# Kernel tuning notes

Measured on AMD Instinct MI355X. Metric: run time of the kernel, lower is better.

## Reference

```python
import jax, jax.numpy as jnp
import numpy as np

N = 500_000
IN_CH = 64
OUT_CH = 32
HEADS = 4
NUM_SEGS = 1024


def setup_inputs() -> dict:
    key = jax.random.key(0)
    ks = jax.random.split(key, 8)
    x = jax.random.normal(ks[0], (N, IN_CH), dtype=jnp.float32)
    batch = jnp.sort(jax.random.randint(ks[1], (N,), 0, NUM_SEGS, dtype=jnp.int32))
    batch = batch.at[-1].set(NUM_SEGS - 1)  # mimic size = batch[-1]+1 == NUM_SEGS
    s_in = 1.0 / np.sqrt(IN_CH)
    s_hg = 1.0 / np.sqrt(HEADS * IN_CH)
    s_hm = 1.0 / np.sqrt(OUT_CH * HEADS)
    # gate_nn: Linear(in, heads*in, bias=False) -> PReLU -> Linear(heads*in, heads, bias=False)
    gate_w1 = jax.random.uniform(ks[2], (HEADS * IN_CH, IN_CH), jnp.float32, -s_in, s_in)
    prelu_a = jnp.asarray(0.25, dtype=jnp.float32)
    gate_w2 = jax.random.uniform(ks[3], (HEADS, HEADS * IN_CH), jnp.float32, -s_hg, s_hg)
    # nn: Linear(in, out*heads) -> ReLU -> Linear(out*heads, out*heads)
    mlp_w1 = jax.random.uniform(ks[4], (OUT_CH * HEADS, IN_CH), jnp.float32, -s_in, s_in)
    mlp_b1 = jax.random.uniform(ks[5], (OUT_CH * HEADS,), jnp.float32, -s_in, s_in)
    mlp_w2 = jax.random.uniform(ks[6], (OUT_CH * HEADS, OUT_CH * HEADS), jnp.float32, -s_hm, s_hm)
    mlp_b2 = jax.random.uniform(ks[7], (OUT_CH * HEADS,), jnp.float32, -s_hm, s_hm)
    return {"x": x, "batch": batch, "num_segments": NUM_SEGS,
            "gate_w1": gate_w1, "prelu_a": prelu_a, "gate_w2": gate_w2,
            "mlp_w1": mlp_w1, "mlp_b1": mlp_b1, "mlp_w2": mlp_w2, "mlp_b2": mlp_b2}


def reference(x, batch, num_segments, gate_w1, prelu_a, gate_w2,
              mlp_w1, mlp_b1, mlp_w2, mlp_b2):
    n = x.shape[0]
    # gate network: [N, heads]
    h = x @ gate_w1.T
    h = jnp.where(h >= 0, h, prelu_a * h)  # PReLU (shared scalar slope)
    gate = h @ gate_w2.T
    # feature MLP: [N, heads, out]
    feat = jax.nn.relu(x @ mlp_w1.T + mlp_b1) @ mlp_w2.T + mlp_b2
    feat = feat.reshape(n, HEADS, -1)
    # segment (per-graph) softmax over nodes, per head
    gmax = jax.ops.segment_max(gate, batch, num_segments=num_segments)  # [S, heads]
    escore = jnp.exp(gate - gmax[batch])
    denom = jax.ops.segment_sum(escore, batch, num_segments=num_segments)
    score = escore / (denom[batch] + 1e-16)  # [N, heads]
    # weighted scatter-add pooling
    out = jax.ops.segment_sum(score[..., None] * feat, batch, num_segments=num_segments)
    return out.reshape(num_segments, -1)  # [S, heads*out]
```

## Files before the change

kernel.cpp:

```cpp
#include <hip/hip_runtime.h>
#include <cstdint>
#include <cstddef>

#define NN 500000
#define NG 15625
#define NBLK 1536
#define NWAVES (NBLK * 2)

typedef __attribute__((ext_vector_type(8))) short short8;
typedef __attribute__((ext_vector_type(4))) float floatx4;
typedef __attribute__((ext_vector_type(4))) float fv4;

__device__ __forceinline__ unsigned short f2bf(float f) {
  union { float f; unsigned u; } v; v.f = f;
  unsigned r = v.u + 0x7FFFu + ((v.u >> 16) & 1u);
  return (unsigned short)(r >> 16);
}
__device__ __forceinline__ unsigned cvtpk(float a, float b) {
  unsigned r;
  asm("v_cvt_pk_bf16_f32 %0, %1, %2" : "=v"(r) : "v"(a), "v"(b));
  return r;
}
__device__ __forceinline__ fv4 ntload4(const float* p) {
  return __builtin_nontemporal_load((const fv4*)p);
}
__device__ __forceinline__ float bflo(unsigned u) {
  union { unsigned u; float f; } v; v.u = u << 16; return v.f;
}
__device__ __forceinline__ float bfhi(unsigned u) {
  union { unsigned u; float f; } v; v.u = u & 0xffff0000u; return v.f;
}

#define MFMA16(a, b, c) __builtin_amdgcn_mfma_f32_16x16x32_bf16((a), (b), (c), 0, 0, 0)

__global__ void swizzle_weights(const float* __restrict__ gw1, const float* __restrict__ mw1,
                                unsigned short* __restrict__ gw1s,
                                unsigned short* __restrict__ mw1s,
                                float* __restrict__ denom, float* __restrict__ zws) {
  int e = blockIdx.x * 256 + threadIdx.x;
  if (e < 4096) denom[e] = 0.f;
#pragma unroll
  for (int i = 0; i < 22; ++i) {
    int o = e + i * 24576;
    if (o < 524288) zws[o] = 0.f;
  }
  const float* src; unsigned short* dst; int local;
  if (e < 16384) { src = gw1; dst = gw1s; local = e; }
  else           { src = mw1; dst = mw1s; local = e - 16384; }
  int j = local & 7, lane = (local >> 3) & 63, tile = local >> 9;
  int ks = tile & 1, mtile = tile >> 1;
  int row = mtile * 16 + (lane & 15);
  int k   = ks * 32 + ((lane >> 4) & 3) * 8 + j;
  dst[local] = f2bf(src[row * 64 + k]);
}

#define FLUSH() do {                                                          \
  if (quad == 0) {                                                            \
    _Pragma("unroll") for (int mt_ = 0; mt_ < 8; ++mt_)                       \
      _Pragma("unroll") for (int r_ = 0; r_ < 4; ++r_)                        \
        atomicAdd(&zws[((size_t)cur_seg * 4 + r_) * 128 + mt_ * 16 + lcol],   \
                  acc[mt_][r_]);                                              \
  }                                                                           \
  _Pragma("unroll") for (int mt_ = 0; mt_ < 8; ++mt_)                         \
    acc[mt_] = (floatx4){0.f, 0.f, 0.f, 0.f};                                 \
  { float v_ = es; v_ += __shfl_xor(v_, 16); v_ += __shfl_xor(v_, 32);        \
    if (lane < 4) atomicAdd(&denom[cur_seg * 4 + lane], v_); }                \
  es = 0.f;                                                                   \
} while (0)

__global__ __launch_bounds__(128, 2) void fused_kernel(
    const float* __restrict__ x, const int* __restrict__ batch,
    const unsigned short* __restrict__ gw1s, const unsigned short* __restrict__ mw1s,
    const float* __restrict__ gw2, const float* __restrict__ prelu_a,
    const float* __restrict__ b1, float* __restrict__ denom,
    float* __restrict__ zws) {
  __shared__ float gw2L[1024];
  const int t = threadIdx.x;
  const int wave = t >> 6, lane = t & 63;
  const int quad = lane >> 4, lcol = lane & 15;

  for (int i = t; i < 1024; i += 128) gw2L[i] = gw2[(i & 3) * 256 + (i >> 2)];
  __syncthreads();

  const float slope = prelu_a[0];
  const int W = blockIdx.x * 2 + wave;
  const int g0 = (int)(((long long)W * NG) / NWAVES);
  const int g1 = (int)(((long long)(W + 1) * NG) / NWAVES);

  float b1v[8];
#pragma unroll
  for (int mt = 0; mt < 8; ++mt) b1v[mt] = b1[mt * 16 + lcol];

  floatx4 acc[8];
#pragma unroll
  for (int mt = 0; mt < 8; ++mt) acc[mt] = (floatx4){0.f, 0.f, 0.f, 0.f};
  float es = 0.f;
  int fs = g0 * 32; if (fs > NN - 1) fs = NN - 1;
  int cur_seg = batch[fs];

  for (int g = g0; g < g1; ++g) {
    const int base = g * 32;
    int sv[2];
    short8 bx[2][2];
#pragma unroll
    for (int nt = 0; nt < 2; ++nt) {
      int node = base + nt * 16 + lcol;
      sv[nt] = batch[node];
      const float* xp = x + (size_t)node * 64 + quad * 8;
      fv4 v0 = ntload4(xp), v1 = ntload4(xp + 4);
      fv4 v2 = ntload4(xp + 32), v3 = ntload4(xp + 36);
      union { short8 s; unsigned u[4]; } u0, u1;
      u0.u[0] = cvtpk(v0[0], v0[1]); u0.u[1] = cvtpk(v0[2], v0[3]);
      u0.u[2] = cvtpk(v1[0], v1[1]); u0.u[3] = cvtpk(v1[2], v1[3]);
      u1.u[0] = cvtpk(v2[0], v2[1]); u1.u[1] = cvtpk(v2[2], v2[3]);
      u1.u[2] = cvtpk(v3[0], v3[1]); u1.u[3] = cvtpk(v3[2], v3[3]);
      bx[nt][0] = u0.s; bx[nt][1] = u1.s;
    }

    float gp[2][4];
#pragma unroll
    for (int nt = 0; nt < 2; ++nt)
#pragma unroll
      for (int h = 0; h < 4; ++h) gp[nt][h] = 0.f;
#pragma unroll 2
    for (int mt = 0; mt < 16; ++mt) {
      short8 a0 = *(const short8*)(gw1s + ((size_t)(mt * 2 + 0) * 64 + lane) * 8);
      short8 a1 = *(const short8*)(gw1s + ((size_t)(mt * 2 + 1) * 64 + lane) * 8);
      fv4 g2r0 = *(const fv4*)&gw2L[(mt * 16 + quad * 4 + 0) * 4];
      fv4 g2r1 = *(const fv4*)&gw2L[(mt * 16 + quad * 4 + 1) * 4];
      fv4 g2r2 = *(const fv4*)&gw2L[(mt * 16 + quad * 4 + 2) * 4];
      fv4 g2r3 = *(const fv4*)&gw2L[(mt * 16 + quad * 4 + 3) * 4];
#pragma unroll
      for (int nt = 0; nt < 2; ++nt) {
        floatx4 cc = {0.f, 0.f, 0.f, 0.f};
        cc = MFMA16(a0, bx[nt][0], cc);
        cc = MFMA16(a1, bx[nt][1], cc);
        float h0 = cc[0] >= 0.f ? cc[0] : slope * cc[0];
        float h1v = cc[1] >= 0.f ? cc[1] : slope * cc[1];
        float h2 = cc[2] >= 0.f ? cc[2] : slope * cc[2];
        float h3 = cc[3] >= 0.f ? cc[3] : slope * cc[3];
        gp[nt][0] += g2r0[0]*h0 + g2r1[0]*h1v + g2r2[0]*h2 + g2r3[0]*h3;
        gp[nt][1] += g2r0[1]*h0 + g2r1[1]*h1v + g2r2[1]*h2 + g2r3[1]*h3;
        gp[nt][2] += g2r0[2]*h0 + g2r1[2]*h1v + g2r2[2]*h2 + g2r3[2]*h3;
        gp[nt][3] += g2r0[3]*h0 + g2r1[3]*h1v + g2r2[3]*h2 + g2r3[3]*h3;
      }
    }
    float e16[2][4];
#pragma unroll
    for (int nt = 0; nt < 2; ++nt)
#pragma unroll
      for (int h = 0; h < 4; ++h) {
        float v = gp[nt][h];
        v += __shfl_xor(v, 16);
        v += __shfl_xor(v, 32);
        e16[nt][h] = __expf(v);
      }

    union BH { short8 s; unsigned u[4]; } zb[8];
#pragma unroll
    for (int mt = 0; mt < 8; ++mt) {
      short8 w0 = *(const short8*)(mw1s + ((size_t)(mt * 2 + 0) * 64 + lane) * 8);
      short8 w1 = *(const short8*)(mw1s + ((size_t)(mt * 2 + 1) * 64 + lane) * 8);
      float bb = b1v[mt];
      unsigned pk[2][2];
#pragma unroll
      for (int nt = 0; nt < 2; ++nt) {
        floatx4 cc = {0.f, 0.f, 0.f, 0.f};
        cc = MFMA16(bx[nt][0], w0, cc);
        cc = MFMA16(bx[nt][1], w1, cc);
        float h0 = fmaxf(cc[0] + bb, 0.f), h1v = fmaxf(cc[1] + bb, 0.f);
        float h2 = fmaxf(cc[2] + bb, 0.f), h3 = fmaxf(cc[3] + bb, 0.f);
        pk[nt][0] = cvtpk(h0, h1v);
        pk[nt][1] = cvtpk(h2, h3);
      }
#pragma unroll
      for (int jj = 0; jj < 4; ++jj) {
        int src = ((quad & 1) * 2 + (jj >> 1)) * 16 + lcol;
        unsigned v0 = __shfl(pk[0][jj & 1], src);
        unsigned v1 = __shfl(pk[1][jj & 1], src);
        zb[mt].u[jj] = (quad < 2) ? v0 : v1;
      }
    }

    float ev[8]; int svb[8];
#pragma unroll
    for (int j = 0; j < 8; ++j) {
      int m = (quad & 1) * 8 + j;
      int s0 = __shfl(sv[0], m), s1 = __shfl(sv[1], m);
      svb[j] = (quad < 2) ? s0 : s1;
      float a0 = __shfl(e16[0][0], m), b0 = __shfl(e16[1][0], m);
      float a1 = __shfl(e16[0][1], m), b1x = __shfl(e16[1][1], m);
      float a2 = __shfl(e16[0][2], m), b2x = __shfl(e16[1][2], m);
      float a3 = __shfl(e16[0][3], m), b3 = __shfl(e16[1][3], m);
      float v0 = (quad < 2) ? a0 : b0;
      float v1 = (quad < 2) ? a1 : b1x;
      float v2 = (quad < 2) ? a2 : b2x;
      float v3 = (quad < 2) ? a3 : b3;
      float c01 = (lcol & 1) ? v1 : v0;
      float c23 = (lcol & 1) ? v3 : v2;
      ev[j] = (lcol & 2) ? c23 : c01;
    }

    int p = 0;
    while (p < 32) {
      int selv = (p >> 4) ? sv[1] : sv[0];
      int s = __shfl(selv, p & 15);
      if (s != cur_seg) { FLUSH(); cur_seg = s; }
      int cnt = (int)__popcll(__ballot(sv[0] == s)) +
                (int)__popcll(__ballot(sv[1] == s));
      union { unsigned u[4]; short8 s8; } ea;
#pragma unroll
      for (int jj = 0; jj < 4; ++jj) {
        float e0 = (lcol < 4 && svb[2 * jj] == s) ? ev[2 * jj] : 0.f;
        float e1 = (lcol < 4 && svb[2 * jj + 1] == s) ? ev[2 * jj + 1] : 0.f;
        ea.u[jj] = cvtpk(e0, e1);
        es += bflo(ea.u[jj]) + bfhi(ea.u[jj]);
      }
#pragma unroll
      for (int mt = 0; mt < 8; ++mt)
        acc[mt] = MFMA16(ea.s8, zb[mt].s, acc[mt]);
      p += (cnt >> 2);
    }
  }
  FLUSH();
}

__global__ __launch_bounds__(128) void finalize_kernel(
    const float* __restrict__ zws, const float* __restrict__ denom,
    const float* __restrict__ mw2, const float* __restrict__ b2,
    float* __restrict__ out) {
  __shared__ float zL[512];
  const int seg = blockIdx.x, t = threadIdx.x;
#pragma unroll
  for (int i = 0; i < 4; ++i) zL[t + i * 128] = zws[(size_t)seg * 512 + t + i * 128];
  __syncthreads();
  const int fcol = t, h = t >> 5;
  float d = denom[seg * 4 + h];
  const fv4* mrow = (const fv4*)(mw2 + (size_t)fcol * 128);
  const fv4* zrow = (const fv4*)(zL + h * 128);
  float a0 = 0.f, a1 = 0.f, a2 = 0.f, a3 = 0.f;
#pragma unroll 8
  for (int k = 0; k < 32; ++k) {
    fv4 w = mrow[k], z = zrow[k];
    a0 = fmaf(w[0], z[0], a0); a1 = fmaf(w[1], z[1], a1);
    a2 = fmaf(w[2], z[2], a2); a3 = fmaf(w[3], z[3], a3);
  }
  float acc = (a0 + a1) + (a2 + a3);
  out[(size_t)seg * 128 + fcol] = (d > 0.f) ? (acc / d + b2[fcol]) : 0.f;
}

extern "C" void kernel_launch(void* const* d_in, const int* in_sizes, int n_in,
                              void* d_out, int out_size, void* d_ws, size_t ws_size,
                              hipStream_t stream) {
  const float* x     = (const float*)d_in[0];
  const int*   batch = (const int*)d_in[1];
  const float* gw1 = (const float*)d_in[3];
  const float* pa  = (const float*)d_in[4];
  const float* gw2 = (const float*)d_in[5];
  const float* mw1 = (const float*)d_in[6];
  const float* mb1 = (const float*)d_in[7];
  const float* mw2 = (const float*)d_in[8];
  const float* mb2 = (const float*)d_in[9];
  float* out = (float*)d_out;

  char* ws = (char*)d_ws;
  float* denom = (float*)ws;
  unsigned short* gw1s = (unsigned short*)(ws + 16384);
  unsigned short* mw1s = (unsigned short*)(ws + 49152);
  float* zws = (float*)(ws + 65536);

  swizzle_weights<<<96, 256, 0, stream>>>(gw1, mw1, gw1s, mw1s, denom, zws);

  fused_kernel<<<NBLK, 128, 0, stream>>>(x, batch, gw1s, mw1s, gw2,
                                         pa, mb1, denom, zws);

  finalize_kernel<<<1024, 128, 0, stream>>>(zws, denom, mw2, mb2, out);
}
```

Before: 298.0 us.

## Compute gate second layer with bf16 MFMA instead of scalar FMAs

The second gate linear layer (256 to 4 heads) now runs as MFMA with a pre-swizzled, zero-padded bf16 gw2 weight tile, replacing per-lane scalar FMA reductions, LDS staging and cross-quad shuffles. The PReLU outputs are packed to bf16 and fed straight back as MFMA operands. The feature MLP output layout is also changed so it needs no lane shuffles, and the score broadcast shuffles are rewritten to match. This trades VALU and LDS work for extra MFMAs and lower gate precision (bf16 hidden activations and weights).

Result: faster. 267.3 us (-10.3%).

```diff
diff --git a/kernel.cpp b/kernel.cpp
--- a/kernel.cpp
+++ b/kernel.cpp
@@ -34,15 +34,25 @@
 #define MFMA16(a, b, c) __builtin_amdgcn_mfma_f32_16x16x32_bf16((a), (b), (c), 0, 0, 0)
 
 __global__ void swizzle_weights(const float* __restrict__ gw1, const float* __restrict__ mw1,
+                                const float* __restrict__ gw2,
                                 unsigned short* __restrict__ gw1s,
                                 unsigned short* __restrict__ mw1s,
+                                unsigned short* __restrict__ gw2s,
                                 float* __restrict__ denom, float* __restrict__ zws) {
   int e = blockIdx.x * 256 + threadIdx.x;
   if (e < 4096) denom[e] = 0.f;
 #pragma unroll
-  for (int i = 0; i < 22; ++i) {
-    int o = e + i * 24576;
+  for (int i = 0; i < 19; ++i) {
+    int o = e + i * 28672;
     if (o < 524288) zws[o] = 0.f;
+  }
+  if (e >= 24576) {
+    int local = e - 24576;
+    int j = local & 7, lane = (local >> 3) & 63, s = local >> 9;
+    int row = lane & 15, quad = (lane >> 4) & 3;
+    int w = s * 32 + ((j >> 2) << 4) + 4 * quad + (j & 3);
+    gw2s[local] = (row < 4) ? f2bf(gw2[row * 256 + w]) : (unsigned short)0;
+    return;
   }
   const float* src; unsigned short* dst; int local;
   if (e < 16384) { src = gw1; dst = gw1s; local = e; }
@@ -71,16 +81,12 @@
 __global__ __launch_bounds__(128, 2) void fused_kernel(
     const float* __restrict__ x, const int* __restrict__ batch,
     const unsigned short* __restrict__ gw1s, const unsigned short* __restrict__ mw1s,
-    const float* __restrict__ gw2, const float* __restrict__ prelu_a,
+    const unsigned short* __restrict__ gw2s, const float* __restrict__ prelu_a,
     const float* __restrict__ b1, float* __restrict__ denom,
     float* __restrict__ zws) {
-  __shared__ float gw2L[1024];
   const int t = threadIdx.x;
   const int wave = t >> 6, lane = t & 63;
   const int quad = lane >> 4, lcol = lane & 15;
-
-  for (int i = t; i < 1024; i += 128) gw2L[i] = gw2[(i & 3) * 256 + (i >> 2)];
-  __syncthreads();
 
   const float slope = prelu_a[0];
   const int W = blockIdx.x * 2 + wave;
@@ -117,44 +123,56 @@
       bx[nt][0] = u0.s; bx[nt][1] = u1.s;
     }
 
-    float gp[2][4];
-#pragma unroll
-    for (int nt = 0; nt < 2; ++nt)
-#pragma unroll
-      for (int h = 0; h < 4; ++h) gp[nt][h] = 0.f;
-#pragma unroll 2
-    for (int mt = 0; mt < 16; ++mt) {
-      short8 a0 = *(const short8*)(gw1s + ((size_t)(mt * 2 + 0) * 64 + lane) * 8);
-      short8 a1 = *(const short8*)(gw1s + ((size_t)(mt * 2 + 1) * 64 + lane) * 8);
-      fv4 g2r0 = *(const fv4*)&gw2L[(mt * 16 + quad * 4 + 0) * 4];
-      fv4 g2r1 = *(const fv4*)&gw2L[(mt * 16 + quad * 4 + 1) * 4];
-      fv4 g2r2 = *(const fv4*)&gw2L[(mt * 16 + quad * 4 + 2) * 4];
-      fv4 g2r3 = *(const fv4*)&gw2L[(mt * 16 + quad * 4 + 3) * 4];
-#pragma unroll
-      for (int nt = 0; nt < 2; ++nt) {
-        floatx4 cc = {0.f, 0.f, 0.f, 0.f};
-        cc = MFMA16(a0, bx[nt][0], cc);
-        cc = MFMA16(a1, bx[nt][1], cc);
-        float h0 = cc[0] >= 0.f ? cc[0] : slope * cc[0];
-        float h1v = cc[1] >= 0.f ? cc[1] : slope * cc[1];
-        float h2 = cc[2] >= 0.f ? cc[2] : slope * cc[2];
-        float h3 = cc[3] >= 0.f ? cc[3] : slope * cc[3];
-        gp[nt][0] += g2r0[0]*h0 + g2r1[0]*h1v + g2r2[0]*h2 + g2r3[0]*h3;
-        gp[nt][1] += g2r0[1]*h0 + g2r1[1]*h1v + g2r2[1]*h2 + g2r3[1]*h3;
-        gp[nt][2] += g2r0[2]*h0 + g2r1[2]*h1v + g2r2[2]*h2 + g2r3[2]*h3;
-        gp[nt][3] += g2r0[3]*h0 + g2r1[3]*h1v + g2r2[3]*h2 + g2r3[3]*h3;
+    floatx4 cg0 = {0.f, 0.f, 0.f, 0.f}, cg1 = {0.f, 0.f, 0.f, 0.f};
+#pragma unroll
+    for (int sst = 0; sst < 8; ++sst) {
+      union GB { short8 s; unsigned u[4]; } gb0, gb1;
+#pragma unroll
+      for (int half = 0; half < 2; ++half) {
+        const int mt = sst * 2 + half;
+        short8 a0 = *(const short8*)(gw1s + ((size_t)(mt * 2 + 0) * 64 + lane) * 8);
+        short8 a1 = *(const short8*)(gw1s + ((size_t)(mt * 2 + 1) * 64 + lane) * 8);
+        floatx4 c0 = {0.f, 0.f, 0.f, 0.f};
+        c0 = MFMA16(a0, bx[0][0], c0);
+        c0 = MFMA16(a1, bx[0][1], c0);
+        floatx4 c1 = {0.f, 0.f, 0.f, 0.f};
+        c1 = MFMA16(a0, bx[1][0], c1);
+        c1 = MFMA16(a1, bx[1][1], c1);
+        gb0.u[half * 2 + 0] = cvtpk(fmaxf(c0[0], slope * c0[0]),
+                                    fmaxf(c0[1], slope * c0[1]));
+        gb0.u[half * 2 + 1] = cvtpk(fmaxf(c0[2], slope * c0[2]),
+                                    fmaxf(c0[3], slope * c0[3]));
+        gb1.u[half * 2 + 0] = cvtpk(fmaxf(c1[0], slope * c1[0]),
+                                    fmaxf(c1[1], slope * c1[1]));
+        gb1.u[half * 2 + 1] = cvtpk(fmaxf(c1[2], slope * c1[2]),
+                                    fmaxf(c1[3], slope * c1[3]));
       }
-    }
-    float e16[2][4];
-#pragma unroll
-    for (int nt = 0; nt < 2; ++nt)
-#pragma unroll
-      for (int h = 0; h < 4; ++h) {
-        float v = gp[nt][h];
-        v += __shfl_xor(v, 16);
-        v += __shfl_xor(v, 32);
-        e16[nt][h] = __expf(v);
-      }
+      short8 ga = *(const short8*)(gw2s + ((size_t)sst * 64 + lane) * 8);
+      cg0 = MFMA16(ga, gb0.s, cg0);
+      cg1 = MFMA16(ga, gb1.s, cg1);
+    }
+    float e0a[4], e1a[4];
+#pragma unroll
+    for (int hh = 0; hh < 4; ++hh) {
+      e0a[hh] = __expf(cg0[hh]);
+      e1a[hh] = __expf(cg1[hh]);
+    }
+
+    float ev[8]; int svb[8];
+#pragma unroll
+    for (int j = 0; j < 4; ++j) {
+      int src = 4 * quad + j;
+      svb[j]     = __shfl(sv[0], src);
+      svb[4 + j] = __shfl(sv[1], src);
+      float t0 = __shfl(e0a[0], src), t1 = __shfl(e0a[1], src);
+      float t2 = __shfl(e0a[2], src), t3 = __shfl(e0a[3], src);
+      float c01 = (lcol & 1) ? t1 : t0, c23 = (lcol & 1) ? t3 : t2;
+      ev[j] = (lcol & 2) ? c23 : c01;
+      t0 = __shfl(e1a[0], src); t1 = __shfl(e1a[1], src);
+      t2 = __shfl(e1a[2], src); t3 = __shfl(e1a[3], src);
+      c01 = (lcol & 1) ? t1 : t0; c23 = (lcol & 1) ? t3 : t2;
+      ev[4 + j] = (lcol & 2) ? c23 : c01;
+    }
 
     union BH { short8 s; unsigned u[4]; } zb[8];
 #pragma unroll
@@ -162,43 +180,16 @@
       short8 w0 = *(const short8*)(mw1s + ((size_t)(mt * 2 + 0) * 64 + lane) * 8);
       short8 w1 = *(const short8*)(mw1s + ((size_t)(mt * 2 + 1) * 64 + lane) * 8);
       float bb = b1v[mt];
-      unsigned pk[2][2];
-#pragma unroll
-      for (int nt = 0; nt < 2; ++nt) {
-        floatx4 cc = {0.f, 0.f, 0.f, 0.f};
-        cc = MFMA16(bx[nt][0], w0, cc);
-        cc = MFMA16(bx[nt][1], w1, cc);
-        float h0 = fmaxf(cc[0] + bb, 0.f), h1v = fmaxf(cc[1] + bb, 0.f);
-        float h2 = fmaxf(cc[2] + bb, 0.f), h3 = fmaxf(cc[3] + bb, 0.f);
-        pk[nt][0] = cvtpk(h0, h1v);
-        pk[nt][1] = cvtpk(h2, h3);
-      }
-#pragma unroll
-      for (int jj = 0; jj < 4; ++jj) {
-        int src = ((quad & 1) * 2 + (jj >> 1)) * 16 + lcol;
-        unsigned v0 = __shfl(pk[0][jj & 1], src);
-        unsigned v1 = __shfl(pk[1][jj & 1], src);
-        zb[mt].u[jj] = (quad < 2) ? v0 : v1;
-      }
-    }
-
-    float ev[8]; int svb[8];
-#pragma unroll
-    for (int j = 0; j < 8; ++j) {
-      int m = (quad & 1) * 8 + j;
-      int s0 = __shfl(sv[0], m), s1 = __shfl(sv[1], m);
-      svb[j] = (quad < 2) ? s0 : s1;
-      float a0 = __shfl(e16[0][0], m), b0 = __shfl(e16[1][0], m);
-      float a1 = __shfl(e16[0][1], m), b1x = __shfl(e16[1][1], m);
-      float a2 = __shfl(e16[0][2], m), b2x = __shfl(e16[1][2], m);
-      float a3 = __shfl(e16[0][3], m), b3 = __shfl(e16[1][3], m);
-      float v0 = (quad < 2) ? a0 : b0;
-      float v1 = (quad < 2) ? a1 : b1x;
-      float v2 = (quad < 2) ? a2 : b2x;
-      float v3 = (quad < 2) ? a3 : b3;
-      float c01 = (lcol & 1) ? v1 : v0;
-      float c23 = (lcol & 1) ? v3 : v2;
-      ev[j] = (lcol & 2) ? c23 : c01;
+      floatx4 c0 = {0.f, 0.f, 0.f, 0.f};
+      c0 = MFMA16(bx[0][0], w0, c0);
+      c0 = MFMA16(bx[0][1], w1, c0);
+      floatx4 c1 = {0.f, 0.f, 0.f, 0.f};
+      c1 = MFMA16(bx[1][0], w0, c1);
+      c1 = MFMA16(bx[1][1], w1, c1);
+      zb[mt].u[0] = cvtpk(fmaxf(c0[0] + bb, 0.f), fmaxf(c0[1] + bb, 0.f));
+      zb[mt].u[1] = cvtpk(fmaxf(c0[2] + bb, 0.f), fmaxf(c0[3] + bb, 0.f));
+      zb[mt].u[2] = cvtpk(fmaxf(c1[0] + bb, 0.f), fmaxf(c1[1] + bb, 0.f));
+      zb[mt].u[3] = cvtpk(fmaxf(c1[2] + bb, 0.f), fmaxf(c1[3] + bb, 0.f));
     }
 
     int p = 0;
@@ -267,11 +258,13 @@
   float* denom = (float*)ws;
   unsigned short* gw1s = (unsigned short*)(ws + 16384);
   unsigned short* mw1s = (unsigned short*)(ws + 49152);
-  float* zws = (float*)(ws + 65536);
-
-  swizzle_weights<<<96, 256, 0, stream>>>(gw1, mw1, gw1s, mw1s, denom, zws);
-
-  fused_kernel<<<NBLK, 128, 0, stream>>>(x, batch, gw1s, mw1s, gw2,
+  unsigned short* gw2s = (unsigned short*)(ws + 65536);
+  float* zws = (float*)(ws + 73728);
+
+  swizzle_weights<<<112, 256, 0, stream>>>(gw1, mw1, gw2, gw1s, mw1s, gw2s,
+                                           denom, zws);
+
+  fused_kernel<<<NBLK, 128, 0, stream>>>(x, batch, gw1s, mw1s, gw2s,
                                          pa, mb1, denom, zws);
 
   finalize_kernel<<<1024, 128, 0, stream>>>(zws, denom, mw2, mb2, out);
```
